# Kernel optimization log

Hardware: AMD Instinct MI355X
Metric: run time of the kernel (lower is better)

Reference implementation:

```python
import jax, jax.numpy as jnp
import numpy as np

N = 50000      # nodes
E = 800000     # edges (avg degree 16)
H = 128        # hidden
ED = 64        # edge_dim
L = 3          # num_layers
LN_EPS = 1e-5


def setup_inputs() -> dict:
    key = jax.random.key(0)
    ks = jax.random.split(key, 12)
    s = jax.random.normal(ks[0], (N, H), dtype=jnp.float32)
    edge_index = jax.random.randint(ks[1], (2, E), 0, N, dtype=jnp.int32)
    edge_attr = jax.random.normal(ks[2], (E, ED), dtype=jnp.float32)
    sc = 0.02
    We = sc * jax.random.normal(ks[3], (L, ED, H), dtype=jnp.float32)
    be = sc * jax.random.normal(ks[4], (L, H), dtype=jnp.float32)
    W1 = sc * jax.random.normal(ks[5], (L, H, H), dtype=jnp.float32)
    b1 = sc * jax.random.normal(ks[6], (L, H), dtype=jnp.float32)
    W2 = sc * jax.random.normal(ks[7], (L, H, H), dtype=jnp.float32)
    b2 = sc * jax.random.normal(ks[8], (L, H), dtype=jnp.float32)
    gamma = jnp.ones((L, H), dtype=jnp.float32)
    beta = jnp.zeros((L, H), dtype=jnp.float32)
    return {"s": s, "edge_index": edge_index, "edge_attr": edge_attr,
            "We": We, "be": be, "W1": W1, "b1": b1, "W2": W2, "b2": b2,
            "gamma": gamma, "beta": beta}


def reference(s, edge_index, edge_attr, We, be, W1, b1, W2, b2, gamma, beta):
    src = edge_index[0]  # j (source of message)
    dst = edge_index[1]  # i (target / aggregation index)
    for l in range(L):
        # GINEConv: message = relu(x_j + Lin(edge_attr)); sum-aggregate; eps=0
        e = edge_attr @ We[l] + be[l]                       # [E, H]
        msg = jax.nn.relu(s[src] + e)                       # [E, H] gather + fuse
        agg = jax.ops.segment_sum(msg, dst, num_segments=N)  # [N, H] scatter-add
        h = s + agg                                         # (1+eps)*x + aggr, eps=0
        h = jax.nn.silu(h @ W1[l] + b1[l]) @ W2[l] + b2[l]   # GINE MLP
        s = s + h                                           # residual
        mu = jnp.mean(s, axis=-1, keepdims=True)
        var = jnp.var(s, axis=-1, keepdims=True)
        s = (s - mu) * jax.lax.rsqrt(var + LN_EPS) * gamma[l] + beta[l]
        s = jax.nn.silu(s)
        # dropout p=0.0 / eval mode -> identity
    return s
```

## Files before the change

### kernel.cpp

```cpp
#include <hip/hip_runtime.h>
#include <hip/hip_bf16.h>

#define HH 128
#define EDD 64
#define NLAYER 3
#define LN_EPS 1e-5f
#define LROW 136

typedef __attribute__((ext_vector_type(8))) __bf16 bf16x8;
typedef __attribute__((ext_vector_type(4))) float f32x4;

static __device__ __forceinline__ float bf2f(unsigned short u) {
    return __uint_as_float(((unsigned)u) << 16);
}
static __device__ __forceinline__ unsigned short f2bf(float f) {
    return __builtin_bit_cast(unsigned short, (__bf16)f);
}
static __device__ __forceinline__ float silu(float x) {
    return x / (1.f + __expf(-x));
}

__global__ __launch_bounds__(256) void hist_kernel(
    const int* __restrict__ dst, int* __restrict__ cnt, int E)
{
    for (int e = blockIdx.x * blockDim.x + threadIdx.x; e < E;
         e += gridDim.x * blockDim.x)
        atomicAdd(&cnt[dst[e]], 1);
}

__global__ __launch_bounds__(1024) void scan_kernel(
    const int* __restrict__ cnt, int* __restrict__ off, int N)
{
    __shared__ int ls[1024];
    const int t = threadIdx.x;
    const int C = (N + 1023) >> 10;
    const int lo = t * C;
    const int hi = min(lo + C, N);
    int sum = 0;
    for (int i = lo; i < hi; ++i) sum += cnt[i];
    ls[t] = sum;
    __syncthreads();
    for (int d = 1; d < 1024; d <<= 1) {
        int v = (t >= d) ? ls[t - d] : 0;
        __syncthreads();
        ls[t] += v;
        __syncthreads();
    }
    int excl = (t == 0) ? 0 : ls[t - 1];
    for (int i = lo; i < hi; ++i) { off[i] = excl; excl += cnt[i]; }
    if (t == 1023) off[N] = ls[1023];
}

__global__ __launch_bounds__(256) void scatter2_kernel(
    const int* __restrict__ src, const int* __restrict__ dst,
    int* __restrict__ cursor, int* __restrict__ src_s,
    int* __restrict__ eid_s, int E)
{
    if (blockIdx.x == 0 && threadIdx.x < 16) {
        src_s[E + threadIdx.x] = 0;
        eid_s[E + threadIdx.x] = 0;
    }
    for (int e = blockIdx.x * blockDim.x + threadIdx.x; e < E;
         e += gridDim.x * blockDim.x) {
        const int pos = atomicAdd(&cursor[dst[e]], 1);
        src_s[pos] = src[e];
        eid_s[pos] = e;
    }
}

__global__ __launch_bounds__(256) void conv_ea(
    const float* __restrict__ ea, unsigned short* __restrict__ ea_b,
    long long total4)
{
    for (long long i = blockIdx.x * 256LL + threadIdx.x; i < total4;
         i += gridDim.x * 256LL) {
        const float4 v = reinterpret_cast<const float4*>(ea)[i];
        ushort4 o;
        o.x = f2bf(v.x); o.y = f2bf(v.y); o.z = f2bf(v.z); o.w = f2bf(v.w);
        reinterpret_cast<ushort4*>(ea_b)[i] = o;
    }
}

__global__ __launch_bounds__(256) void conv_s(
    const float* __restrict__ s0, unsigned int* __restrict__ sbp,
    long long total4)
{
    for (long long i = blockIdx.x * 256LL + threadIdx.x; i < total4;
         i += gridDim.x * 256LL) {
        const float4 v = reinterpret_cast<const float4*>(s0)[i];
        const unsigned a = (unsigned)f2bf(v.x) | ((unsigned)f2bf(v.y) << 16);
        const unsigned b = (unsigned)f2bf(v.z) | ((unsigned)f2bf(v.w) << 16);
        reinterpret_cast<uint2*>(sbp)[i] = make_uint2(a, b);
    }
}

__global__ void prep_we(const float* __restrict__ We, bf16x8* __restrict__ WeB)
{
    const int t = blockIdx.x * blockDim.x + threadIdx.x;
    if (t >= NLAYER * 16 * 64) return;
    const int lane  = t & 63;
    const int frag  = (t >> 6) & 15;
    const int layer = t >> 10;
    const int kt = frag >> 3, ct = frag & 7;
    const int col = ct * 16 + (lane & 15);
    const int k0  = kt * 32 + (lane >> 4) * 8;
    bf16x8 v;
    #pragma unroll
    for (int j = 0; j < 8; ++j)
        v[j] = (__bf16)We[(long long)layer * EDD * HH + (k0 + j) * HH + col];
    WeB[t] = v;
}

__global__ void prep_w128(const float* __restrict__ W, bf16x8* __restrict__ WB)
{
    const int t = blockIdx.x * blockDim.x + threadIdx.x;
    if (t >= NLAYER * 32 * 64) return;
    const int lane  = t & 63;
    const int frag  = (t >> 6) & 31;
    const int layer = t >> 11;
    const int kt = frag >> 3, ct = frag & 7;
    const int col = ct * 16 + (lane & 15);
    const int k0  = kt * 32 + (lane >> 4) * 8;
    bf16x8 v;
    #pragma unroll
    for (int j = 0; j < 8; ++j)
        v[j] = (__bf16)W[(long long)layer * HH * HH + (k0 + j) * HH + col];
    WB[t] = v;
}

__global__ __launch_bounds__(256) void gine_agg_mfma(
    const float* __restrict__ s,
    const unsigned short* __restrict__ sb,
    const int* __restrict__ src_s,
    const int* __restrict__ eid_s,
    const int* __restrict__ off,
    const unsigned short* __restrict__ ea_b,
    const bf16x8* __restrict__ WeB,
    const float* __restrict__ be,
    unsigned short* __restrict__ hb16,
    int N)
{
    __shared__ unsigned short lsb[16 * LROW];

    const int tid  = threadIdx.x;
    const int wave = tid >> 6;
    const int lane = tid & 63;
    const int lmod = lane & 15;
    const int ldiv = lane >> 4;

    const bf16x8 wb00 = WeB[(0 * 8 + 2 * wave    ) * 64 + lane];
    const bf16x8 wb01 = WeB[(0 * 8 + 2 * wave + 1) * 64 + lane];
    const bf16x8 wb10 = WeB[(1 * 8 + 2 * wave    ) * 64 + lane];
    const bf16x8 wb11 = WeB[(1 * 8 + 2 * wave + 1) * 64 + lane];

    const int col0 = (2 * wave) * 16 + lmod;
    const int col1 = col0 + 16;
    const float bev0 = be[col0];
    const float bev1 = be[col1];

    const int stg_row = tid >> 4;
    const int stg_seg = tid & 15;

    for (int n = blockIdx.x; n < N; n += gridDim.x) {
        const int p0 = off[n], p1 = off[n + 1];
        float acc0 = 0.f, acc1 = 0.f;

        for (int p = p0; p < p1; p += 16) {
            const int rem = p1 - p;

            const int snode = src_s[p + stg_row];
            const uint4 sv4 = *reinterpret_cast<const uint4*>(
                &sb[(long long)snode * HH + stg_seg * 8]);

            __syncthreads();
            *reinterpret_cast<uint4*>(&lsb[stg_row * LROW + stg_seg * 8]) = sv4;

            const int rowid = eid_s[p + lmod];
            const unsigned short* arow = ea_b + (long long)rowid * EDD + ldiv * 8;
            const bf16x8 a0 = *reinterpret_cast<const bf16x8*>(arow);
            const bf16x8 a1 = *reinterpret_cast<const bf16x8*>(arow + 32);

            f32x4 c0 = {0.f, 0.f, 0.f, 0.f};
            f32x4 c1 = {0.f, 0.f, 0.f, 0.f};
            c0 = __builtin_amdgcn_mfma_f32_16x16x32_bf16(a0, wb00, c0, 0, 0, 0);
            c0 = __builtin_amdgcn_mfma_f32_16x16x32_bf16(a1, wb10, c0, 0, 0, 0);
            c1 = __builtin_amdgcn_mfma_f32_16x16x32_bf16(a0, wb01, c1, 0, 0, 0);
            c1 = __builtin_amdgcn_mfma_f32_16x16x32_bf16(a1, wb11, c1, 0, 0, 0);

            __syncthreads();

            #pragma unroll
            for (int r = 0; r < 4; ++r) {
                if (ldiv * 4 + r < rem) {
                    const int lr = (ldiv * 4 + r) * LROW;
                    acc0 += fmaxf(bf2f(lsb[lr + col0]) + c0[r] + bev0, 0.f);
                    acc1 += fmaxf(bf2f(lsb[lr + col1]) + c1[r] + bev1, 0.f);
                }
            }
        }

        acc0 += __shfl_xor(acc0, 16, 64);
        acc0 += __shfl_xor(acc0, 32, 64);
        acc1 += __shfl_xor(acc1, 16, 64);
        acc1 += __shfl_xor(acc1, 32, 64);

        if (ldiv < 2) {
            const int col = (ldiv == 0) ? col0 : col1;
            const float a = (ldiv == 0) ? acc0 : acc1;
            hb16[(long long)n * HH + col] =
                f2bf(s[(long long)n * HH + col] + a);
        }
    }
}

__global__ __launch_bounds__(256) void gine_mlp1(
    const unsigned short* __restrict__ h16,
    const bf16x8* __restrict__ W1B,
    const float* __restrict__ b1,
    unsigned short* __restrict__ t1,
    int N)
{
    const int wave = threadIdx.x >> 6;
    const int lane = threadIdx.x & 63;
    const int lmod = lane & 15;
    const int ldiv = lane >> 4;

    bf16x8 wf[4][2];
    #pragma unroll
    for (int kt = 0; kt < 4; ++kt) {
        wf[kt][0] = W1B[(kt * 8 + 2 * wave    ) * 64 + lane];
        wf[kt][1] = W1B[(kt * 8 + 2 * wave + 1) * 64 + lane];
    }
    float4 bv[2];
    bv[0] = *reinterpret_cast<const float4*>(&b1[(2 * wave)     * 16 + ldiv * 4]);
    bv[1] = *reinterpret_cast<const float4*>(&b1[(2 * wave + 1) * 16 + ldiv * 4]);

    const int ntiles = (N + 15) >> 4;
    for (int t = blockIdx.x; t < ntiles; t += gridDim.x) {
        const int node = t * 16 + lmod;
        const long long hb = (long long)min(node, N - 1) * HH;

        f32x4 c0 = {0.f, 0.f, 0.f, 0.f};
        f32x4 c1 = {0.f, 0.f, 0.f, 0.f};
        #pragma unroll
        for (int kt = 0; kt < 4; ++kt) {
            const bf16x8 hf = *reinterpret_cast<const bf16x8*>(
                &h16[hb + kt * 32 + ldiv * 8]);
            c0 = __builtin_amdgcn_mfma_f32_16x16x32_bf16(wf[kt][0], hf, c0, 0, 0, 0);
            c1 = __builtin_amdgcn_mfma_f32_16x16x32_bf16(wf[kt][1], hf, c1, 0, 0, 0);
        }

        if (node < N) {
            const long long tb = (long long)node * HH;
            #pragma unroll
            for (int ctl = 0; ctl < 2; ++ctl) {
                const f32x4 cc = ctl ? c1 : c0;
                const int oc0 = (2 * wave + ctl) * 16 + ldiv * 4;
                const float v0 = silu(cc[0] + (ctl ? bv[1].x : bv[0].x));
                const float v1 = silu(cc[1] + (ctl ? bv[1].y : bv[0].y));
                const float v2 = silu(cc[2] + (ctl ? bv[1].z : bv[0].z));
                const float v3 = silu(cc[3] + (ctl ? bv[1].w : bv[0].w));
                uint2 pk;
                pk.x = (unsigned)f2bf(v0) | ((unsigned)f2bf(v1) << 16);
                pk.y = (unsigned)f2bf(v2) | ((unsigned)f2bf(v3) << 16);
                *reinterpret_cast<uint2*>(&t1[tb + oc0]) = pk;
            }
        }
    }
}

__global__ __launch_bounds__(256) void gine_mlp2(
    const float* __restrict__ s_in,
    const unsigned short* __restrict__ t1,
    const bf16x8* __restrict__ W2B,
    const float* __restrict__ b2,
    const float* __restrict__ gamma,
    const float* __restrict__ beta,
    float* __restrict__ s_out,
    unsigned short* __restrict__ sb_out,
    int N)
{
    __shared__ float2 red[4][16];

    const int wave = threadIdx.x >> 6;
    const int lane = threadIdx.x & 63;
    const int lmod = lane & 15;
    const int ldiv = lane >> 4;

    bf16x8 wf[4][2];
    #pragma unroll
    for (int kt = 0; kt < 4; ++kt) {
        wf[kt][0] = W2B[(kt * 8 + 2 * wave    ) * 64 + lane];
        wf[kt][1] = W2B[(kt * 8 + 2 * wave + 1) * 64 + lane];
    }
    float4 bv[2], gv[2], ev[2];
    #pragma unroll
    for (int ctl = 0; ctl < 2; ++ctl) {
        const int oc0 = (2 * wave + ctl) * 16 + ldiv * 4;
        bv[ctl] = *reinterpret_cast<const float4*>(&b2[oc0]);
        gv[ctl] = *reinterpret_cast<const float4*>(&gamma[oc0]);
        ev[ctl] = *reinterpret_cast<const float4*>(&beta[oc0]);
    }

    const int ntiles = (N + 15) >> 4;
    for (int t = blockIdx.x; t < ntiles; t += gridDim.x) {
        const int node = t * 16 + lmod;
        const long long nb = (long long)min(node, N - 1) * HH;

        f32x4 c0 = {0.f, 0.f, 0.f, 0.f};
        f32x4 c1 = {0.f, 0.f, 0.f, 0.f};
        #pragma unroll
        for (int kt = 0; kt < 4; ++kt) {
            const bf16x8 tf = *reinterpret_cast<const bf16x8*>(
                &t1[nb + kt * 32 + ldiv * 8]);
            c0 = __builtin_amdgcn_mfma_f32_16x16x32_bf16(wf[kt][0], tf, c0, 0, 0, 0);
            c1 = __builtin_amdgcn_mfma_f32_16x16x32_bf16(wf[kt][1], tf, c1, 0, 0, 0);
        }

        float v[2][4];
        float sum = 0.f, ssq = 0.f;
        #pragma unroll
        for (int ctl = 0; ctl < 2; ++ctl) {
            const int oc0 = (2 * wave + ctl) * 16 + ldiv * 4;
            const float4 sv = *reinterpret_cast<const float4*>(&s_in[nb + oc0]);
            const f32x4 cc = ctl ? c1 : c0;
            v[ctl][0] = sv.x + cc[0] + bv[ctl].x;
            v[ctl][1] = sv.y + cc[1] + bv[ctl].y;
            v[ctl][2] = sv.z + cc[2] + bv[ctl].z;
            v[ctl][3] = sv.w + cc[3] + bv[ctl].w;
            #pragma unroll
            for (int r = 0; r < 4; ++r) { sum += v[ctl][r]; ssq += v[ctl][r] * v[ctl][r]; }
        }
        sum += __shfl_xor(sum, 16, 64); sum += __shfl_xor(sum, 32, 64);
        ssq += __shfl_xor(ssq, 16, 64); ssq += __shfl_xor(ssq, 32, 64);
        if (ldiv == 0) red[wave][lmod] = make_float2(sum, ssq);
        __syncthreads();
        float ts = 0.f, tq = 0.f;
        #pragma unroll
        for (int w = 0; w < 4; ++w) {
            const float2 rr = red[w][lmod];
            ts += rr.x; tq += rr.y;
        }
        __syncthreads();

        const float mu = ts * (1.0f / HH);
        const float var = tq * (1.0f / HH) - mu * mu;
        const float rs = rsqrtf(var + LN_EPS);

        if (node < N) {
            #pragma unroll
            for (int ctl = 0; ctl < 2; ++ctl) {
                const int oc0 = (2 * wave + ctl) * 16 + ldiv * 4;
                float o[4];
                o[0] = silu((v[ctl][0] - mu) * rs * gv[ctl].x + ev[ctl].x);
                o[1] = silu((v[ctl][1] - mu) * rs * gv[ctl].y + ev[ctl].y);
                o[2] = silu((v[ctl][2] - mu) * rs * gv[ctl].z + ev[ctl].z);
                o[3] = silu((v[ctl][3] - mu) * rs * gv[ctl].w + ev[ctl].w);
                *reinterpret_cast<float4*>(&s_out[nb + oc0]) =
                    make_float4(o[0], o[1], o[2], o[3]);
                uint2 pk;
                pk.x = (unsigned)f2bf(o[0]) | ((unsigned)f2bf(o[1]) << 16);
                pk.y = (unsigned)f2bf(o[2]) | ((unsigned)f2bf(o[3]) << 16);
                *reinterpret_cast<uint2*>(&sb_out[nb + oc0]) = pk;
            }
        }
    }
}

extern "C" void kernel_launch(void* const* d_in, const int* in_sizes, int n_in,
                              void* d_out, int out_size, void* d_ws, size_t ws_size,
                              hipStream_t stream) {
    const float* s0  = (const float*)d_in[0];
    const int*   ei  = (const int*)  d_in[1];
    const float* ea  = (const float*)d_in[2];
    const float* We  = (const float*)d_in[3];
    const float* be  = (const float*)d_in[4];
    const float* W1  = (const float*)d_in[5];
    const float* b1  = (const float*)d_in[6];
    const float* W2  = (const float*)d_in[7];
    const float* b2  = (const float*)d_in[8];
    const float* gm  = (const float*)d_in[9];
    const float* bt  = (const float*)d_in[10];

    const int NH = in_sizes[0];
    const int N  = NH / HH;
    const int E  = in_sizes[1] / 2;
    const int* src = ei;
    const int* dst = ei + E;

    float*          sbuf  = (float*)d_ws;
    unsigned short* sb    = (unsigned short*)(sbuf + NH);
    unsigned short* t1b   = sb + NH;
    unsigned short* hb16  = t1b + NH;
    unsigned short* ea_b  = hb16 + NH;
    bf16x8*         WeB   = (bf16x8*)(ea_b + (size_t)E * EDD);
    bf16x8*         W1B   = WeB + NLAYER * 16 * 64;
    bf16x8*         W2B   = W1B + NLAYER * 32 * 64;
    int*            src_s = (int*)(W2B + NLAYER * 32 * 64);
    int*            eid_s = src_s + (E + 16);
    int*            off   = eid_s + (E + 16);
    int*            cursor= off + (N + 1);

    hipMemcpyAsync(sbuf, s0, sizeof(float) * NH, hipMemcpyDeviceToDevice, stream);

    hipMemsetAsync(cursor, 0, sizeof(int) * N, stream);
    hist_kernel<<<1024, 256, 0, stream>>>(dst, cursor, E);
    scan_kernel<<<1, 1024, 0, stream>>>(cursor, off, N);
    hipMemcpyAsync(cursor, off, sizeof(int) * N, hipMemcpyDeviceToDevice, stream);
    scatter2_kernel<<<1024, 256, 0, stream>>>(src, dst, cursor, src_s, eid_s, E);
    conv_ea<<<2048, 256, 0, stream>>>(ea, ea_b, (long long)E * EDD / 4);
    conv_s<<<1024, 256, 0, stream>>>(s0, (unsigned int*)sb, (long long)NH / 4);
    prep_we<<<12, 256, 0, stream>>>(We, WeB);
    prep_w128<<<24, 256, 0, stream>>>(W1, W1B);
    prep_w128<<<24, 256, 0, stream>>>(W2, W2B);

    for (int l = 0; l < NLAYER; ++l) {
        gine_agg_mfma<<<4096, 256, 0, stream>>>(sbuf, sb, src_s, eid_s, off, ea_b,
                                                WeB + (size_t)l * 16 * 64,
                                                be + l * HH, hb16, N);
        gine_mlp1<<<1024, 256, 0, stream>>>(hb16,
                                            W1B + (size_t)l * 32 * 64,
                                            b1 + l * HH, t1b, N);
        float* sout = (l == NLAYER - 1) ? (float*)d_out : sbuf;
        gine_mlp2<<<1024, 256, 0, stream>>>(sbuf, t1b,
                                            W2B + (size_t)l * 32 * 64,
                                            b2 + l * HH,
                                            gm + l * HH, bt + l * HH,
                                            sout, sb, N);
    }
}
```

Before: 736.1 us.

## Fuse MLP kernels via LDS and process two nodes per aggregation block

The two MLP kernels are merged into one. The intermediate SiLU activation now stays in LDS instead of making a round trip through a global bf16 buffer, which also removes one launch per layer. The aggregation kernel now handles two destination nodes per block, with two waves per node each covering 64 columns. This is meant to raise utilisation on low-degree nodes, but it pays for the longer of the two nodes' edge lists. The fused MLP holds both weight sets in registers, which may reduce occupancy.

```diff
diff --git a/kernel.cpp b/kernel.cpp
--- a/kernel.cpp
+++ b/kernel.cpp
@@ -138,168 +138,137 @@
     const bf16x8* __restrict__ WeB,
     const float* __restrict__ be,
     unsigned short* __restrict__ hb16,
-    int N)
-{
-    __shared__ unsigned short lsb[16 * LROW];
+    int N, int E)
+{
+    __shared__ unsigned short lsb[2][16 * LROW];
 
     const int tid  = threadIdx.x;
     const int wave = tid >> 6;
+    const int half = wave & 1;
+    const int slot = wave >> 1;
     const int lane = tid & 63;
     const int lmod = lane & 15;
     const int ldiv = lane >> 4;
 
-    const bf16x8 wb00 = WeB[(0 * 8 + 2 * wave    ) * 64 + lane];
-    const bf16x8 wb01 = WeB[(0 * 8 + 2 * wave + 1) * 64 + lane];
-    const bf16x8 wb10 = WeB[(1 * 8 + 2 * wave    ) * 64 + lane];
-    const bf16x8 wb11 = WeB[(1 * 8 + 2 * wave + 1) * 64 + lane];
-
-    const int col0 = (2 * wave) * 16 + lmod;
-    const int col1 = col0 + 16;
-    const float bev0 = be[col0];
-    const float bev1 = be[col1];
-
-    const int stg_row = tid >> 4;
-    const int stg_seg = tid & 15;
-
-    for (int n = blockIdx.x; n < N; n += gridDim.x) {
-        const int p0 = off[n], p1 = off[n + 1];
-        float acc0 = 0.f, acc1 = 0.f;
-
-        for (int p = p0; p < p1; p += 16) {
+    bf16x8 wb0[4], wb1[4];
+    #pragma unroll
+    for (int c = 0; c < 4; ++c) {
+        wb0[c] = WeB[(0 * 8 + half * 4 + c) * 64 + lane];
+        wb1[c] = WeB[(1 * 8 + half * 4 + c) * 64 + lane];
+    }
+    float bev[4];
+    #pragma unroll
+    for (int c = 0; c < 4; ++c) bev[c] = be[(half * 4 + c) * 16 + lmod];
+
+    const int st_slot = tid >> 7;
+    const int st_row  = (tid >> 3) & 15;
+    const int st_sp   = tid & 7;
+
+    for (int base = blockIdx.x * 2; base < N; base += gridDim.x * 2) {
+        const int n0 = base;
+        const int n1 = (base + 1 < N) ? base + 1 : base;
+        const int q0 = off[n0], q0e = off[n0 + 1];
+        const int q1 = off[n1], q1e = off[n1 + 1];
+        const int iters = max((q0e - q0 + 15) >> 4, (q1e - q1 + 15) >> 4);
+
+        const int myn = slot ? n1 : n0;
+        const int p0  = slot ? q1 : q0;
+        const int p1  = slot ? q1e : q0e;
+        const int sp0 = st_slot ? q1 : q0;
+
+        float acc[4] = {0.f, 0.f, 0.f, 0.f};
+
+        for (int it = 0; it < iters; ++it) {
+            const int sidx  = min(sp0 + it * 16 + st_row, E + 15);
+            const int snode = src_s[sidx];
+            const unsigned short* srow = &sb[(long long)snode * HH + st_sp * 16];
+            const uint4 sva = *reinterpret_cast<const uint4*>(srow);
+            const uint4 svb = *reinterpret_cast<const uint4*>(srow + 8);
+
+            __syncthreads();
+            unsigned short* drow = &lsb[st_slot][st_row * LROW + st_sp * 16];
+            *reinterpret_cast<uint4*>(drow)     = sva;
+            *reinterpret_cast<uint4*>(drow + 8) = svb;
+
+            const int p   = p0 + it * 16;
             const int rem = p1 - p;
-
-            const int snode = src_s[p + stg_row];
-            const uint4 sv4 = *reinterpret_cast<const uint4*>(
-                &sb[(long long)snode * HH + stg_seg * 8]);
-
-            __syncthreads();
-            *reinterpret_cast<uint4*>(&lsb[stg_row * LROW + stg_seg * 8]) = sv4;
-
-            const int rowid = eid_s[p + lmod];
+            const int rowid = eid_s[min(p + lmod, E + 15)];
             const unsigned short* arow = ea_b + (long long)rowid * EDD + ldiv * 8;
             const bf16x8 a0 = *reinterpret_cast<const bf16x8*>(arow);
             const bf16x8 a1 = *reinterpret_cast<const bf16x8*>(arow + 32);
 
-            f32x4 c0 = {0.f, 0.f, 0.f, 0.f};
-            f32x4 c1 = {0.f, 0.f, 0.f, 0.f};
-            c0 = __builtin_amdgcn_mfma_f32_16x16x32_bf16(a0, wb00, c0, 0, 0, 0);
-            c0 = __builtin_amdgcn_mfma_f32_16x16x32_bf16(a1, wb10, c0, 0, 0, 0);
-            c1 = __builtin_amdgcn_mfma_f32_16x16x32_bf16(a0, wb01, c1, 0, 0, 0);
-            c1 = __builtin_amdgcn_mfma_f32_16x16x32_bf16(a1, wb11, c1, 0, 0, 0);
+            f32x4 cf[4];
+            #pragma unroll
+            for (int c = 0; c < 4; ++c) {
+                f32x4 z = {0.f, 0.f, 0.f, 0.f};
+                z = __builtin_amdgcn_mfma_f32_16x16x32_bf16(a0, wb0[c], z, 0, 0, 0);
+                z = __builtin_amdgcn_mfma_f32_16x16x32_bf16(a1, wb1[c], z, 0, 0, 0);
+                cf[c] = z;
+            }
 
             __syncthreads();
 
             #pragma unroll
             for (int r = 0; r < 4; ++r) {
                 if (ldiv * 4 + r < rem) {
-                    const int lr = (ldiv * 4 + r) * LROW;
-                    acc0 += fmaxf(bf2f(lsb[lr + col0]) + c0[r] + bev0, 0.f);
-                    acc1 += fmaxf(bf2f(lsb[lr + col1]) + c1[r] + bev1, 0.f);
+                    const unsigned short* lr = &lsb[slot][(ldiv * 4 + r) * LROW];
+                    #pragma unroll
+                    for (int c = 0; c < 4; ++c) {
+                        acc[c] += fmaxf(
+                            bf2f(lr[(half * 4 + c) * 16 + lmod]) + cf[c][r] + bev[c],
+                            0.f);
+                    }
                 }
             }
         }
 
-        acc0 += __shfl_xor(acc0, 16, 64);
-        acc0 += __shfl_xor(acc0, 32, 64);
-        acc1 += __shfl_xor(acc1, 16, 64);
-        acc1 += __shfl_xor(acc1, 32, 64);
-
-        if (ldiv < 2) {
-            const int col = (ldiv == 0) ? col0 : col1;
-            const float a = (ldiv == 0) ? acc0 : acc1;
-            hb16[(long long)n * HH + col] =
-                f2bf(s[(long long)n * HH + col] + a);
-        }
-    }
-}
-
-__global__ __launch_bounds__(256) void gine_mlp1(
+        #pragma unroll
+        for (int c = 0; c < 4; ++c) {
+            acc[c] += __shfl_xor(acc[c], 16, 64);
+            acc[c] += __shfl_xor(acc[c], 32, 64);
+        }
+        const float av = (ldiv == 0) ? acc[0] : (ldiv == 1) ? acc[1]
+                       : (ldiv == 2) ? acc[2] : acc[3];
+        const int col = (half * 4 + ldiv) * 16 + lmod;
+        const long long nb = (long long)myn * HH;
+        hb16[nb + col] = f2bf(s[nb + col] + av);
+    }
+}
+
+__global__ __launch_bounds__(256) void gine_mlp(
+    const float* __restrict__ s_in,
     const unsigned short* __restrict__ h16,
-    const bf16x8* __restrict__ W1B,
-    const float* __restrict__ b1,
-    unsigned short* __restrict__ t1,
+    const bf16x8* __restrict__ W1B, const float* __restrict__ b1,
+    const bf16x8* __restrict__ W2B, const float* __restrict__ b2,
+    const float* __restrict__ gamma, const float* __restrict__ beta,
+    float* __restrict__ s_out,
+    unsigned short* __restrict__ sb_out,
     int N)
 {
+    __shared__ unsigned short t1t[16 * LROW];
+    __shared__ float2 red[4][16];
+
     const int wave = threadIdx.x >> 6;
     const int lane = threadIdx.x & 63;
     const int lmod = lane & 15;
     const int ldiv = lane >> 4;
 
-    bf16x8 wf[4][2];
+    bf16x8 wf1[4][2], wf2[4][2];
     #pragma unroll
     for (int kt = 0; kt < 4; ++kt) {
-        wf[kt][0] = W1B[(kt * 8 + 2 * wave    ) * 64 + lane];
-        wf[kt][1] = W1B[(kt * 8 + 2 * wave + 1) * 64 + lane];
-    }
-    float4 bv[2];
-    bv[0] = *reinterpret_cast<const float4*>(&b1[(2 * wave)     * 16 + ldiv * 4]);
-    bv[1] = *reinterpret_cast<const float4*>(&b1[(2 * wave + 1) * 16 + ldiv * 4]);
-
-    const int ntiles = (N + 15) >> 4;
-    for (int t = blockIdx.x; t < ntiles; t += gridDim.x) {
-        const int node = t * 16 + lmod;
-        const long long hb = (long long)min(node, N - 1) * HH;
-
-        f32x4 c0 = {0.f, 0.f, 0.f, 0.f};
-        f32x4 c1 = {0.f, 0.f, 0.f, 0.f};
-        #pragma unroll
-        for (int kt = 0; kt < 4; ++kt) {
-            const bf16x8 hf = *reinterpret_cast<const bf16x8*>(
-                &h16[hb + kt * 32 + ldiv * 8]);
-            c0 = __builtin_amdgcn_mfma_f32_16x16x32_bf16(wf[kt][0], hf, c0, 0, 0, 0);
-            c1 = __builtin_amdgcn_mfma_f32_16x16x32_bf16(wf[kt][1], hf, c1, 0, 0, 0);
-        }
-
-        if (node < N) {
-            const long long tb = (long long)node * HH;
-            #pragma unroll
-            for (int ctl = 0; ctl < 2; ++ctl) {
-                const f32x4 cc = ctl ? c1 : c0;
-                const int oc0 = (2 * wave + ctl) * 16 + ldiv * 4;
-                const float v0 = silu(cc[0] + (ctl ? bv[1].x : bv[0].x));
-                const float v1 = silu(cc[1] + (ctl ? bv[1].y : bv[0].y));
-                const float v2 = silu(cc[2] + (ctl ? bv[1].z : bv[0].z));
-                const float v3 = silu(cc[3] + (ctl ? bv[1].w : bv[0].w));
-                uint2 pk;
-                pk.x = (unsigned)f2bf(v0) | ((unsigned)f2bf(v1) << 16);
-                pk.y = (unsigned)f2bf(v2) | ((unsigned)f2bf(v3) << 16);
-                *reinterpret_cast<uint2*>(&t1[tb + oc0]) = pk;
-            }
-        }
-    }
-}
-
-__global__ __launch_bounds__(256) void gine_mlp2(
-    const float* __restrict__ s_in,
-    const unsigned short* __restrict__ t1,
-    const bf16x8* __restrict__ W2B,
-    const float* __restrict__ b2,
-    const float* __restrict__ gamma,
-    const float* __restrict__ beta,
-    float* __restrict__ s_out,
-    unsigned short* __restrict__ sb_out,
-    int N)
-{
-    __shared__ float2 red[4][16];
-
-    const int wave = threadIdx.x >> 6;
-    const int lane = threadIdx.x & 63;
-    const int lmod = lane & 15;
-    const int ldiv = lane >> 4;
-
-    bf16x8 wf[4][2];
-    #pragma unroll
-    for (int kt = 0; kt < 4; ++kt) {
-        wf[kt][0] = W2B[(kt * 8 + 2 * wave    ) * 64 + lane];
-        wf[kt][1] = W2B[(kt * 8 + 2 * wave + 1) * 64 + lane];
-    }
-    float4 bv[2], gv[2], ev[2];
+        wf1[kt][0] = W1B[(kt * 8 + 2 * wave    ) * 64 + lane];
+        wf1[kt][1] = W1B[(kt * 8 + 2 * wave + 1) * 64 + lane];
+        wf2[kt][0] = W2B[(kt * 8 + 2 * wave    ) * 64 + lane];
+        wf2[kt][1] = W2B[(kt * 8 + 2 * wave + 1) * 64 + lane];
+    }
+    float4 b1v[2], b2v[2], gv[2], ev[2];
     #pragma unroll
     for (int ctl = 0; ctl < 2; ++ctl) {
         const int oc0 = (2 * wave + ctl) * 16 + ldiv * 4;
-        bv[ctl] = *reinterpret_cast<const float4*>(&b2[oc0]);
-        gv[ctl] = *reinterpret_cast<const float4*>(&gamma[oc0]);
-        ev[ctl] = *reinterpret_cast<const float4*>(&beta[oc0]);
+        b1v[ctl] = *reinterpret_cast<const float4*>(&b1[oc0]);
+        b2v[ctl] = *reinterpret_cast<const float4*>(&b2[oc0]);
+        gv[ctl]  = *reinterpret_cast<const float4*>(&gamma[oc0]);
+        ev[ctl]  = *reinterpret_cast<const float4*>(&beta[oc0]);
     }
 
     const int ntiles = (N + 15) >> 4;
@@ -311,10 +280,33 @@
         f32x4 c1 = {0.f, 0.f, 0.f, 0.f};
         #pragma unroll
         for (int kt = 0; kt < 4; ++kt) {
+            const bf16x8 hf = *reinterpret_cast<const bf16x8*>(
+                &h16[nb + kt * 32 + ldiv * 8]);
+            c0 = __builtin_amdgcn_mfma_f32_16x16x32_bf16(wf1[kt][0], hf, c0, 0, 0, 0);
+            c1 = __builtin_amdgcn_mfma_f32_16x16x32_bf16(wf1[kt][1], hf, c1, 0, 0, 0);
+        }
+        #pragma unroll
+        for (int ctl = 0; ctl < 2; ++ctl) {
+            const f32x4 cc = ctl ? c1 : c0;
+            const float4 bb = ctl ? b1v[1] : b1v[0];
+            uint2 pk;
+            pk.x = (unsigned)f2bf(silu(cc[0] + bb.x)) |
+                   ((unsigned)f2bf(silu(cc[1] + bb.y)) << 16);
+            pk.y = (unsigned)f2bf(silu(cc[2] + bb.z)) |
+                   ((unsigned)f2bf(silu(cc[3] + bb.w)) << 16);
+            const int oc0 = (2 * wave + ctl) * 16 + ldiv * 4;
+            *reinterpret_cast<uint2*>(&t1t[lmod * LROW + oc0]) = pk;
+        }
+        __syncthreads();
+
+        f32x4 d0 = {0.f, 0.f, 0.f, 0.f};
+        f32x4 d1 = {0.f, 0.f, 0.f, 0.f};
+        #pragma unroll
+        for (int kt = 0; kt < 4; ++kt) {
             const bf16x8 tf = *reinterpret_cast<const bf16x8*>(
-                &t1[nb + kt * 32 + ldiv * 8]);
-            c0 = __builtin_amdgcn_mfma_f32_16x16x32_bf16(wf[kt][0], tf, c0, 0, 0, 0);
-            c1 = __builtin_amdgcn_mfma_f32_16x16x32_bf16(wf[kt][1], tf, c1, 0, 0, 0);
+                &t1t[lmod * LROW + kt * 32 + ldiv * 8]);
+            d0 = __builtin_amdgcn_mfma_f32_16x16x32_bf16(wf2[kt][0], tf, d0, 0, 0, 0);
+            d1 = __builtin_amdgcn_mfma_f32_16x16x32_bf16(wf2[kt][1], tf, d1, 0, 0, 0);
         }
 
         float v[2][4];
@@ -323,11 +315,12 @@
         for (int ctl = 0; ctl < 2; ++ctl) {
             const int oc0 = (2 * wave + ctl) * 16 + ldiv * 4;
             const float4 sv = *reinterpret_cast<const float4*>(&s_in[nb + oc0]);
-            const f32x4 cc = ctl ? c1 : c0;
-            v[ctl][0] = sv.x + cc[0] + bv[ctl].x;
-            v[ctl][1] = sv.y + cc[1] + bv[ctl].y;
-            v[ctl][2] = sv.z + cc[2] + bv[ctl].z;
-            v[ctl][3] = sv.w + cc[3] + bv[ctl].w;
+            const f32x4 dd = ctl ? d1 : d0;
+            const float4 bb = ctl ? b2v[1] : b2v[0];
+            v[ctl][0] = sv.x + dd[0] + bb.x;
+            v[ctl][1] = sv.y + dd[1] + bb.y;
+            v[ctl][2] = sv.z + dd[2] + bb.z;
+            v[ctl][3] = sv.w + dd[3] + bb.w;
             #pragma unroll
             for (int r = 0; r < 4; ++r) { sum += v[ctl][r]; ssq += v[ctl][r] * v[ctl][r]; }
         }
@@ -390,8 +383,7 @@
 
     float*          sbuf  = (float*)d_ws;
     unsigned short* sb    = (unsigned short*)(sbuf + NH);
-    unsigned short* t1b   = sb + NH;
-    unsigned short* hb16  = t1b + NH;
+    unsigned short* hb16  = sb + NH;
     unsigned short* ea_b  = hb16 + NH;
     bf16x8*         WeB   = (bf16x8*)(ea_b + (size_t)E * EDD);
     bf16x8*         W1B   = WeB + NLAYER * 16 * 64;
@@ -417,15 +409,12 @@
     for (int l = 0; l < NLAYER; ++l) {
         gine_agg_mfma<<<4096, 256, 0, stream>>>(sbuf, sb, src_s, eid_s, off, ea_b,
                                                 WeB + (size_t)l * 16 * 64,
-                                                be + l * HH, hb16, N);
-        gine_mlp1<<<1024, 256, 0, stream>>>(hb16,
-                                            W1B + (size_t)l * 32 * 64,
-                                            b1 + l * HH, t1b, N);
+                                                be + l * HH, hb16, N, E);
         float* sout = (l == NLAYER - 1) ? (float*)d_out : sbuf;
-        gine_mlp2<<<1024, 256, 0, stream>>>(sbuf, t1b,
-                                            W2B + (size_t)l * 32 * 64,
-                                            b2 + l * HH,
-                                            gm + l * HH, bt + l * HH,
-                                            sout, sb, N);
-    }
-}
+        gine_mlp<<<2048, 256, 0, stream>>>(sbuf, hb16,
+                                           W1B + (size_t)l * 32 * 64, b1 + l * HH,
+                                           W2B + (size_t)l * 32 * 64, b2 + l * HH,
+                                           gm + l * HH, bt + l * HH,
+                                           sout, sb, N);
+    }
+}
```

Measured after the change: 652.4 us. -11.4%, faster.
